# Performance work log

Hardware: AMD Instinct MI355X
Metric: run time of the kernel (lower is better)

## Reference

```python
import jax, jax.numpy as jnp
import numpy as np
from jax import lax


def _lstm_layer(x, Wih, Whh, bih, bhh):
    # x: [B, T, D_in]; PyTorch gate order: i, f, g, o. Returns all hidden states [B, T, H].
    B = x.shape[0]
    H = Whh.shape[1]
    bias = bih + bhh
    # Precompute input projections for all timesteps: [T, B, 4H]
    xg = jnp.einsum('btd,gd->tbg', x, Wih) + bias

    def step(carry, xg_t):
        h, c = carry
        gates = xg_t + h @ Whh.T  # [B, 4H]
        i, f, g, o = jnp.split(gates, 4, axis=-1)
        i = jax.nn.sigmoid(i)
        f = jax.nn.sigmoid(f)
        g = jnp.tanh(g)
        o = jax.nn.sigmoid(o)
        c = f * c + i * g
        h = o * jnp.tanh(c)
        return (h, c), h

    h0 = jnp.zeros((B, H), dtype=x.dtype)
    c0 = jnp.zeros((B, H), dtype=x.dtype)
    (_, _), hs = lax.scan(step, (h0, c0), xg)  # hs: [T, B, H]
    return hs.transpose(1, 0, 2)


def setup_inputs() -> dict:
    key = jax.random.key(0)
    ks = jax.random.split(key, 13)
    B, T, D = 4096, 128, 32
    H1, H2 = 64, 32
    s = lambda n: 1.0 / np.sqrt(n)
    return {
        'x': jax.random.normal(ks[0], (B, T, D), jnp.float32),
        'Wih1': jax.random.uniform(ks[1], (4 * H1, D), jnp.float32, -s(H1), s(H1)),
        'Whh1': jax.random.uniform(ks[2], (4 * H1, H1), jnp.float32, -s(H1), s(H1)),
        'bih1': jax.random.uniform(ks[3], (4 * H1,), jnp.float32, -s(H1), s(H1)),
        'bhh1': jax.random.uniform(ks[4], (4 * H1,), jnp.float32, -s(H1), s(H1)),
        'Wih2': jax.random.uniform(ks[5], (4 * H2, H1), jnp.float32, -s(H2), s(H2)),
        'Whh2': jax.random.uniform(ks[6], (4 * H2, H2), jnp.float32, -s(H2), s(H2)),
        'bih2': jax.random.uniform(ks[7], (4 * H2,), jnp.float32, -s(H2), s(H2)),
        'bhh2': jax.random.uniform(ks[8], (4 * H2,), jnp.float32, -s(H2), s(H2)),
        'fc1_w': jax.random.uniform(ks[9], (16, H2), jnp.float32, -s(H2), s(H2)),
        'fc1_b': jax.random.uniform(ks[10], (16,), jnp.float32, -s(H2), s(H2)),
        'fc2_w': jax.random.uniform(ks[11], (1, 16), jnp.float32, -0.25, 0.25),
        'fc2_b': jax.random.uniform(ks[12], (1,), jnp.float32, -0.25, 0.25),
    }


def reference(x, Wih1, Whh1, bih1, bhh1, Wih2, Whh2, bih2, bhh2, fc1_w, fc1_b, fc2_w, fc2_b):
    out = _lstm_layer(x, Wih1, Whh1, bih1, bhh1)        # [B, T, H1]; dropout = identity (eval)
    out = _lstm_layer(out, Wih2, Whh2, bih2, bhh2)       # [B, T, H2]
    last = out[:, -1, :]                                  # [B, H2]
    h = jax.nn.relu(last @ fc1_w.T + fc1_b)               # [B, 16]
    return h @ fc2_w.T + fc2_b                            # [B, 1]
```

## Files before the change

kernel.cpp:

```cpp
#include <hip/hip_runtime.h>


typedef _Float16 f16;
typedef f16 h2f __attribute__((ext_vector_type(2)));
typedef f16 h8f __attribute__((ext_vector_type(8)));

constexpr int Tt      = 128;
constexpr int NB      = 8;
constexpr int THREADS = 256;

struct __align__(16) Smem {
  float scr[8192];
  h2f h1p[2][32][8];
  h2f h2p[2][16][8];
  h2f xsp[2][16][8];
};

static_assert(sizeof(Smem) <= 80 * 1024, "need 2 blocks/CU");

__device__ __forceinline__ float frcp(float x)   { return __builtin_amdgcn_rcpf(x); }
__device__ __forceinline__ float fsig(float x)   { return frcp(1.0f + __expf(-x)); }
__device__ __forceinline__ float ftanh_(float x) { return 1.0f - 2.0f * frcp(1.0f + __expf(2.0f * x)); }

template<int P>
__device__ __forceinline__ float swz(float v) {
  return __int_as_float(__builtin_amdgcn_ds_swizzle(__float_as_int(v), P));
}

__device__ __forceinline__ h2f pack2(float a, float b) {
  h2f r; r[0] = (f16)a; r[1] = (f16)b; return r;
}

__global__ __launch_bounds__(THREADS, 2)
void lstm_fused(const float* __restrict__ x,
                const float* __restrict__ Wih1, const float* __restrict__ Whh1,
                const float* __restrict__ bih1, const float* __restrict__ bhh1,
                const float* __restrict__ Wih2, const float* __restrict__ Whh2,
                const float* __restrict__ bih2, const float* __restrict__ bhh2,
                const float* __restrict__ fc1w, const float* __restrict__ fc1b,
                const float* __restrict__ fc2w, const float* __restrict__ fc2b,
                float* __restrict__ out)
{
  __shared__ Smem s;
  const int tid = threadIdx.x;
  const int b0  = blockIdx.x * NB;

  const int ks1 = tid & 3;
  const int u1  = tid >> 2;
  const int ks2 = tid & 7;
  const int u2  = tid >> 3;

  h2f w1[12][4];
  h2f w2[6][4];

  auto stage = [&](const float* g, int n) {
    for (int e = tid * 4; e < n; e += THREADS * 4)
      *(float4*)&s.scr[e] = *(const float4*)&g[e];
  };

  stage(Wih1, 8192);
  __syncthreads();
#pragma unroll
  for (int j = 0; j < 4; ++j) {
    int col = 2 * (ks1 + 4 * j);
#pragma unroll
    for (int g = 0; g < 4; ++g)
      w1[j][g] = pack2(s.scr[(g * 64 + u1) * 32 + col],
                       s.scr[(g * 64 + u1) * 32 + col + 1]);
  }
  __syncthreads();

  stage(Whh1, 8192);
  __syncthreads();
#pragma unroll
  for (int j = 4; j < 12; ++j) {
    int col = 2 * (ks1 + 4 * j) - 32;
#pragma unroll
    for (int g = 0; g < 2; ++g)
      w1[j][g] = pack2(s.scr[(g * 64 + u1) * 64 + col],
                       s.scr[(g * 64 + u1) * 64 + col + 1]);
  }
  __syncthreads();

  stage(Whh1 + 8192, 8192);
  __syncthreads();
#pragma unroll
  for (int j = 4; j < 12; ++j) {
    int col = 2 * (ks1 + 4 * j) - 32;
#pragma unroll
    for (int g = 2; g < 4; ++g)
      w1[j][g] = pack2(s.scr[((g - 2) * 64 + u1) * 64 + col],
                       s.scr[((g - 2) * 64 + u1) * 64 + col + 1]);
  }
  __syncthreads();

  stage(Wih2, 8192);
  __syncthreads();
#pragma unroll
  for (int j = 0; j < 4; ++j) {
    int col = 2 * (ks2 + 8 * j);
#pragma unroll
    for (int g = 0; g < 4; ++g)
      w2[j][g] = pack2(s.scr[(g * 32 + u2) * 64 + col],
                       s.scr[(g * 32 + u2) * 64 + col + 1]);
  }
  __syncthreads();

  stage(Whh2, 4096);
  __syncthreads();
#pragma unroll
  for (int j = 4; j < 6; ++j) {
    int col = 2 * (ks2 + 8 * j) - 64;
#pragma unroll
    for (int g = 0; g < 4; ++g)
      w2[j][g] = pack2(s.scr[(g * 32 + u2) * 32 + col],
                       s.scr[(g * 32 + u2) * 32 + col + 1]);
  }

  float bias1[4], bias2[4];
#pragma unroll
  for (int g = 0; g < 4; ++g) {
    bias1[g] = bih1[g * 64 + u1] + bhh1[g * 64 + u1];
    bias2[g] = bih2[g * 32 + u2] + bhh2[g * 32 + u2];
  }

  if (tid < 256) {
    uint* z1 = (uint*)&s.h1p[0][0][0];
    z1[tid] = 0u;
  }
  if (tid < 128) {
    uint* z2 = (uint*)&s.h2p[0][0][0];
    z2[tid] = 0u;
  }

  const int    xb   = tid >> 4;
  const int    xr   = tid & 15;
  const float* xptr = x + (size_t)(b0 + xb) * (Tt * 32) + 2 * xr;
  if (tid < 128) {
    float2 x0 = *(const float2*)xptr;
    s.xsp[0][xr][xb] = pack2(x0.x, x0.y);
  }

  float c1[2] = {0.0f, 0.0f};
  float c2    = 0.0f;

  const bool sA = (ks1 & 1) != 0;
  const bool sB = (ks1 & 2) != 0;
  const bool t0 = (ks2 & 1) != 0;
  const bool t1 = (ks2 & 2) != 0;
  const bool t2 = (ks2 & 4) != 0;

  __syncthreads();

#pragma unroll 1
  for (int t = 0; t < Tt; ++t) {
    const int c = t & 1, n = c ^ 1;

    float2 xpre = make_float2(0.0f, 0.0f);
    if (tid < 128 && t + 1 < Tt) xpre = *(const float2*)(xptr + (size_t)(t + 1) * 32);

    float a[4][8];
#pragma unroll
    for (int g = 0; g < 4; ++g)
#pragma unroll
      for (int b = 0; b < 8; ++b) a[g][b] = 0.0f;

#pragma unroll
    for (int j = 0; j < 12; ++j) {
      const h8f* row = (j < 4) ? (const h8f*)&s.xsp[c][ks1 + 4 * j][0]
                               : (const h8f*)&s.h1p[c][ks1 + 4 * j - 16][0];
      union { h8f v; h2f p[4]; } U0, U1;
      U0.v = row[0];
      U1.v = row[1];
#pragma unroll
      for (int g = 0; g < 4; ++g) {
#pragma unroll
        for (int b = 0; b < 4; ++b)
          a[g][b] = __builtin_amdgcn_fdot2(w1[j][g], U0.p[b], a[g][b], false);
#pragma unroll
        for (int b = 0; b < 4; ++b)
          a[g][4 + b] = __builtin_amdgcn_fdot2(w1[j][g], U1.p[b], a[g][4 + b], false);
      }
    }

    float tot[4][2];
#pragma unroll
    for (int g = 0; g < 4; ++g) {
      float r1[4];
#pragma unroll
      for (int i = 0; i < 4; ++i) {
        float snd  = sA ? a[g][2 * i]     : a[g][2 * i + 1];
        float kept = sA ? a[g][2 * i + 1] : a[g][2 * i];
        r1[i] = kept + swz<0x041F>(snd);
      }
#pragma unroll
      for (int i = 0; i < 2; ++i) {
        float snd  = sB ? r1[2 * i]     : r1[2 * i + 1];
        float kept = sB ? r1[2 * i + 1] : r1[2 * i];
        tot[g][i] = kept + swz<0x081F>(snd);
      }
    }

#pragma unroll
    for (int bb = 0; bb < 2; ++bb) {
      float iv = fsig  (tot[0][bb] + bias1[0]);
      float fv = fsig  (tot[1][bb] + bias1[1]);
      float gv = ftanh_(tot[2][bb] + bias1[2]);
      float ov = fsig  (tot[3][bb] + bias1[3]);
      c1[bb] = fv * c1[bb] + iv * gv;
      float hval = ov * ftanh_(c1[bb]);
      f16* dst = (f16*)&s.h1p[n][u1 >> 1][ks1 + 4 * bb];
      dst[u1 & 1] = (f16)hval;
    }
    __syncthreads();

    if (tid < 128 && t + 1 < Tt) s.xsp[n][xr][xb] = pack2(xpre.x, xpre.y);

    float a2[4][8];
#pragma unroll
    for (int g = 0; g < 4; ++g)
#pragma unroll
      for (int b = 0; b < 8; ++b) a2[g][b] = 0.0f;

#pragma unroll
    for (int j = 0; j < 6; ++j) {
      const h8f* row = (j < 4) ? (const h8f*)&s.h1p[n][ks2 + 8 * j][0]
                               : (const h8f*)&s.h2p[c][ks2 + 8 * j - 32][0];
      union { h8f v; h2f p[4]; } U0, U1;
      U0.v = row[0];
      U1.v = row[1];
#pragma unroll
      for (int g = 0; g < 4; ++g) {
#pragma unroll
        for (int b = 0; b < 4; ++b)
          a2[g][b] = __builtin_amdgcn_fdot2(w2[j][g], U0.p[b], a2[g][b], false);
#pragma unroll
        for (int b = 0; b < 4; ++b)
          a2[g][4 + b] = __builtin_amdgcn_fdot2(w2[j][g], U1.p[b], a2[g][4 + b], false);
      }
    }

    float tot2[4];
#pragma unroll
    for (int g = 0; g < 4; ++g) {
      float r1[4];
#pragma unroll
      for (int i = 0; i < 4; ++i) {
        float snd  = t0 ? a2[g][2 * i]     : a2[g][2 * i + 1];
        float kept = t0 ? a2[g][2 * i + 1] : a2[g][2 * i];
        r1[i] = kept + swz<0x041F>(snd);
      }
      float r2[2];
#pragma unroll
      for (int i = 0; i < 2; ++i) {
        float snd  = t1 ? r1[2 * i]     : r1[2 * i + 1];
        float kept = t1 ? r1[2 * i + 1] : r1[2 * i];
        r2[i] = kept + swz<0x081F>(snd);
      }
      float snd  = t2 ? r2[0] : r2[1];
      float kept = t2 ? r2[1] : r2[0];
      tot2[g] = kept + swz<0x101F>(snd);
    }

    {
      float iv = fsig  (tot2[0] + bias2[0]);
      float fv = fsig  (tot2[1] + bias2[1]);
      float gv = ftanh_(tot2[2] + bias2[2]);
      float ov = fsig  (tot2[3] + bias2[3]);
      c2 = fv * c2 + iv * gv;
      float hval = ov * ftanh_(c2);
      f16* dst = (f16*)&s.h2p[n][u2 >> 1][ks2];
      dst[u2 & 1] = (f16)hval;
    }
    __syncthreads();
  }

  float* fc1out = s.scr;
  if (tid < 128) {
    const int fb = tid >> 4, fu = tid & 15;
    const f16* h2flat = (const f16*)&s.h2p[0][0][0];
    float sacc = fc1b[fu];
#pragma unroll
    for (int k = 0; k < 32; ++k) {
      float hv = (float)h2flat[(k >> 1) * 16 + fb * 2 + (k & 1)];
      sacc = fmaf(fc1w[fu * 32 + k], hv, sacc);
    }
    fc1out[fb * 16 + fu] = fmaxf(sacc, 0.0f);
  }
  __syncthreads();
  if (tid < NB) {
    float o = fc2b[0];
#pragma unroll
    for (int u = 0; u < 16; ++u) o = fmaf(fc2w[u], fc1out[tid * 16 + u], o);
    out[b0 + tid] = o;
  }
}

extern "C" void kernel_launch(void* const* d_in, const int* in_sizes, int n_in,
                              void* d_out, int out_size, void* d_ws, size_t ws_size,
                              hipStream_t stream) {
  const float* x    = (const float*)d_in[0];
  const float* Wih1 = (const float*)d_in[1];
  const float* Whh1 = (const float*)d_in[2];
  const float* bih1 = (const float*)d_in[3];
  const float* bhh1 = (const float*)d_in[4];
  const float* Wih2 = (const float*)d_in[5];
  const float* Whh2 = (const float*)d_in[6];
  const float* bih2 = (const float*)d_in[7];
  const float* bhh2 = (const float*)d_in[8];
  const float* fc1w = (const float*)d_in[9];
  const float* fc1b = (const float*)d_in[10];
  const float* fc2w = (const float*)d_in[11];
  const float* fc2b = (const float*)d_in[12];
  float* out = (float*)d_out;

  hipLaunchKernelGGL(lstm_fused, dim3(4096 / NB), dim3(THREADS), 0, stream,
                     x, Wih1, Whh1, bih1, bhh1,
                     Wih2, Whh2, bih2, bhh2,
                     fc1w, fc1b, fc2w, fc2b, out);
}
```

Baseline: 638.0 us.

## Halve batch per block, preload inputs to shared memory, drop per-step barrier

Each block now handles 4 batch rows instead of 8. Shared memory and launch bounds are resized so 4 blocks fit per CU, and the grid doubles. The whole input sequence for the block is loaded into shared memory as fp16 before the time loop, which removes the per-step global prefetch. The end-of-step barrier is dropped because the double-buffered h1/h2 states and the mid-step barrier already order the accesses. Each thread does half as many dot products per step and the reductions are shortened; the cost is more blocks, more weight staging per batch row, and higher register and occupancy pressure.

```diff
diff --git a/kernel.cpp b/kernel.cpp
--- a/kernel.cpp
+++ b/kernel.cpp
@@ -6,17 +6,17 @@
 typedef f16 h8f __attribute__((ext_vector_type(8)));
 
 constexpr int Tt      = 128;
-constexpr int NB      = 8;
+constexpr int NB      = 4;
 constexpr int THREADS = 256;
 
 struct __align__(16) Smem {
   float scr[8192];
-  h2f h1p[2][32][8];
-  h2f h2p[2][16][8];
-  h2f xsp[2][16][8];
+  h2f h1p[2][32][4];
+  h2f h2p[2][16][4];
+  float fcs[64];
 };
 
-static_assert(sizeof(Smem) <= 80 * 1024, "need 2 blocks/CU");
+static_assert(sizeof(Smem) <= 40 * 1024, "need 4 blocks/CU");
 
 __device__ __forceinline__ float frcp(float x)   { return __builtin_amdgcn_rcpf(x); }
 __device__ __forceinline__ float fsig(float x)   { return frcp(1.0f + __expf(-x)); }
@@ -31,7 +31,7 @@
   h2f r; r[0] = (f16)a; r[1] = (f16)b; return r;
 }
 
-__global__ __launch_bounds__(THREADS, 2)
+__global__ __launch_bounds__(THREADS, 4)
 void lstm_fused(const float* __restrict__ x,
                 const float* __restrict__ Wih1, const float* __restrict__ Whh1,
                 const float* __restrict__ bih1, const float* __restrict__ bhh1,
@@ -116,6 +116,21 @@
       w2[j][g] = pack2(s.scr[(g * 32 + u2) * 32 + col],
                        s.scr[(g * 32 + u2) * 32 + col + 1]);
   }
+  __syncthreads();
+
+  {
+    h2f* xf = (h2f*)s.scr;
+    const int dp = tid & 15;
+    const int t0 = (tid >> 4) & 3;
+    const int xb = tid >> 6;
+    const float* xp = x + (size_t)(b0 + xb) * (Tt * 32) + 2 * dp;
+#pragma unroll 4
+    for (int i = 0; i < 32; ++i) {
+      int t = t0 + 4 * i;
+      float2 v = *(const float2*)(xp + (size_t)t * 32);
+      xf[t * 64 + dp * 4 + xb] = pack2(v.x, v.y);
+    }
+  }
 
   float bias1[4], bias2[4];
 #pragma unroll
@@ -124,31 +139,18 @@
     bias2[g] = bih2[g * 32 + u2] + bhh2[g * 32 + u2];
   }
 
-  if (tid < 256) {
-    uint* z1 = (uint*)&s.h1p[0][0][0];
-    z1[tid] = 0u;
-  }
-  if (tid < 128) {
-    uint* z2 = (uint*)&s.h2p[0][0][0];
-    z2[tid] = 0u;
-  }
-
-  const int    xb   = tid >> 4;
-  const int    xr   = tid & 15;
-  const float* xptr = x + (size_t)(b0 + xb) * (Tt * 32) + 2 * xr;
-  if (tid < 128) {
-    float2 x0 = *(const float2*)xptr;
-    s.xsp[0][xr][xb] = pack2(x0.x, x0.y);
-  }
-
-  float c1[2] = {0.0f, 0.0f};
-  float c2    = 0.0f;
+  if (tid < 128) ((uint*)&s.h1p[0][0][0])[tid] = 0u;
+  if (tid < 64)  ((uint*)&s.h2p[0][0][0])[tid] = 0u;
+
+  float c1 = 0.0f;
+  float c2 = 0.0f;
 
   const bool sA = (ks1 & 1) != 0;
   const bool sB = (ks1 & 2) != 0;
-  const bool t0 = (ks2 & 1) != 0;
-  const bool t1 = (ks2 & 2) != 0;
-  const bool t2 = (ks2 & 4) != 0;
+  const bool t0b = (ks2 & 1) != 0;
+  const bool t1b = (ks2 & 2) != 0;
+
+  const h2f* xf = (const h2f*)s.scr;
 
   __syncthreads();
 
@@ -156,110 +158,82 @@
   for (int t = 0; t < Tt; ++t) {
     const int c = t & 1, n = c ^ 1;
 
-    float2 xpre = make_float2(0.0f, 0.0f);
-    if (tid < 128 && t + 1 < Tt) xpre = *(const float2*)(xptr + (size_t)(t + 1) * 32);
-
-    float a[4][8];
-#pragma unroll
-    for (int g = 0; g < 4; ++g)
-#pragma unroll
-      for (int b = 0; b < 8; ++b) a[g][b] = 0.0f;
+    float a[4][4];
+#pragma unroll
+    for (int g = 0; g < 4; ++g)
+#pragma unroll
+      for (int b = 0; b < 4; ++b) a[g][b] = 0.0f;
 
 #pragma unroll
     for (int j = 0; j < 12; ++j) {
-      const h8f* row = (j < 4) ? (const h8f*)&s.xsp[c][ks1 + 4 * j][0]
-                               : (const h8f*)&s.h1p[c][ks1 + 4 * j - 16][0];
-      union { h8f v; h2f p[4]; } U0, U1;
-      U0.v = row[0];
-      U1.v = row[1];
-#pragma unroll
-      for (int g = 0; g < 4; ++g) {
+      const h8f row = (j < 4) ? *(const h8f*)&xf[t * 64 + (ks1 + 4 * j) * 4]
+                              : *(const h8f*)&s.h1p[c][ks1 + 4 * j - 16][0];
+      union { h8f v; h2f p[4]; } U; U.v = row;
+#pragma unroll
+      for (int g = 0; g < 4; ++g)
 #pragma unroll
         for (int b = 0; b < 4; ++b)
-          a[g][b] = __builtin_amdgcn_fdot2(w1[j][g], U0.p[b], a[g][b], false);
-#pragma unroll
-        for (int b = 0; b < 4; ++b)
-          a[g][4 + b] = __builtin_amdgcn_fdot2(w1[j][g], U1.p[b], a[g][4 + b], false);
-      }
-    }
-
-    float tot[4][2];
+          a[g][b] = __builtin_amdgcn_fdot2(w1[j][g], U.p[b], a[g][b], false);
+    }
+
+    float tot[4];
 #pragma unroll
     for (int g = 0; g < 4; ++g) {
-      float r1[4];
-#pragma unroll
-      for (int i = 0; i < 4; ++i) {
+      float r1[2];
+#pragma unroll
+      for (int i = 0; i < 2; ++i) {
         float snd  = sA ? a[g][2 * i]     : a[g][2 * i + 1];
         float kept = sA ? a[g][2 * i + 1] : a[g][2 * i];
         r1[i] = kept + swz<0x041F>(snd);
       }
+      float snd  = sB ? r1[0] : r1[1];
+      float kept = sB ? r1[1] : r1[0];
+      tot[g] = kept + swz<0x081F>(snd);
+    }
+
+    {
+      float iv = fsig  (tot[0] + bias1[0]);
+      float fv = fsig  (tot[1] + bias1[1]);
+      float gv = ftanh_(tot[2] + bias1[2]);
+      float ov = fsig  (tot[3] + bias1[3]);
+      c1 = fv * c1 + iv * gv;
+      float hval = ov * ftanh_(c1);
+      ((f16*)&s.h1p[n][u1 >> 1][ks1])[u1 & 1] = (f16)hval;
+    }
+    __syncthreads();
+
+    float a2[4][4];
+#pragma unroll
+    for (int g = 0; g < 4; ++g)
+#pragma unroll
+      for (int b = 0; b < 4; ++b) a2[g][b] = 0.0f;
+
+#pragma unroll
+    for (int j = 0; j < 6; ++j) {
+      const h8f row = (j < 4) ? *(const h8f*)&s.h1p[n][ks2 + 8 * j][0]
+                              : *(const h8f*)&s.h2p[c][ks2 + 8 * j - 32][0];
+      union { h8f v; h2f p[4]; } U; U.v = row;
+#pragma unroll
+      for (int g = 0; g < 4; ++g)
+#pragma unroll
+        for (int b = 0; b < 4; ++b)
+          a2[g][b] = __builtin_amdgcn_fdot2(w2[j][g], U.p[b], a2[g][b], false);
+    }
+
+    float tot2[4];
+#pragma unroll
+    for (int g = 0; g < 4; ++g) {
+      float r1[2];
 #pragma unroll
       for (int i = 0; i < 2; ++i) {
-        float snd  = sB ? r1[2 * i]     : r1[2 * i + 1];
-        float kept = sB ? r1[2 * i + 1] : r1[2 * i];
-        tot[g][i] = kept + swz<0x081F>(snd);
-      }
-    }
-
-#pragma unroll
-    for (int bb = 0; bb < 2; ++bb) {
-      float iv = fsig  (tot[0][bb] + bias1[0]);
-      float fv = fsig  (tot[1][bb] + bias1[1]);
-      float gv = ftanh_(tot[2][bb] + bias1[2]);
-      float ov = fsig  (tot[3][bb] + bias1[3]);
-      c1[bb] = fv * c1[bb] + iv * gv;
-      float hval = ov * ftanh_(c1[bb]);
-      f16* dst = (f16*)&s.h1p[n][u1 >> 1][ks1 + 4 * bb];
-      dst[u1 & 1] = (f16)hval;
-    }
-    __syncthreads();
-
-    if (tid < 128 && t + 1 < Tt) s.xsp[n][xr][xb] = pack2(xpre.x, xpre.y);
-
-    float a2[4][8];
-#pragma unroll
-    for (int g = 0; g < 4; ++g)
-#pragma unroll
-      for (int b = 0; b < 8; ++b) a2[g][b] = 0.0f;
-
-#pragma unroll
-    for (int j = 0; j < 6; ++j) {
-      const h8f* row = (j < 4) ? (const h8f*)&s.h1p[n][ks2 + 8 * j][0]
-                               : (const h8f*)&s.h2p[c][ks2 + 8 * j - 32][0];
-      union { h8f v; h2f p[4]; } U0, U1;
-      U0.v = row[0];
-      U1.v = row[1];
-#pragma unroll
-      for (int g = 0; g < 4; ++g) {
-#pragma unroll
-        for (int b = 0; b < 4; ++b)
-          a2[g][b] = __builtin_amdgcn_fdot2(w2[j][g], U0.p[b], a2[g][b], false);
-#pragma unroll
-        for (int b = 0; b < 4; ++b)
-          a2[g][4 + b] = __builtin_amdgcn_fdot2(w2[j][g], U1.p[b], a2[g][4 + b], false);
-      }
-    }
-
-    float tot2[4];
-#pragma unroll
-    for (int g = 0; g < 4; ++g) {
-      float r1[4];
-#pragma unroll
-      for (int i = 0; i < 4; ++i) {
-        float snd  = t0 ? a2[g][2 * i]     : a2[g][2 * i + 1];
-        float kept = t0 ? a2[g][2 * i + 1] : a2[g][2 * i];
+        float snd  = t0b ? a2[g][2 * i]     : a2[g][2 * i + 1];
+        float kept = t0b ? a2[g][2 * i + 1] : a2[g][2 * i];
         r1[i] = kept + swz<0x041F>(snd);
       }
-      float r2[2];
-#pragma unroll
-      for (int i = 0; i < 2; ++i) {
-        float snd  = t1 ? r1[2 * i]     : r1[2 * i + 1];
-        float kept = t1 ? r1[2 * i + 1] : r1[2 * i];
-        r2[i] = kept + swz<0x081F>(snd);
-      }
-      float snd  = t2 ? r2[0] : r2[1];
-      float kept = t2 ? r2[1] : r2[0];
-      tot2[g] = kept + swz<0x101F>(snd);
+      float snd  = t1b ? r1[0] : r1[1];
+      float kept = t1b ? r1[1] : r1[0];
+      float r2 = kept + swz<0x081F>(snd);
+      tot2[g] = r2 + swz<0x101F>(r2);
     }
 
     {
@@ -269,29 +243,27 @@
       float ov = fsig  (tot2[3] + bias2[3]);
       c2 = fv * c2 + iv * gv;
       float hval = ov * ftanh_(c2);
-      f16* dst = (f16*)&s.h2p[n][u2 >> 1][ks2];
-      dst[u2 & 1] = (f16)hval;
-    }
-    __syncthreads();
-  }
-
-  float* fc1out = s.scr;
-  if (tid < 128) {
+      if (ks2 < 4)
+        ((f16*)&s.h2p[n][u2 >> 1][ks2 & 3])[u2 & 1] = (f16)hval;
+    }
+  }
+  __syncthreads();
+
+  if (tid < 64) {
     const int fb = tid >> 4, fu = tid & 15;
-    const f16* h2flat = (const f16*)&s.h2p[0][0][0];
     float sacc = fc1b[fu];
 #pragma unroll
     for (int k = 0; k < 32; ++k) {
-      float hv = (float)h2flat[(k >> 1) * 16 + fb * 2 + (k & 1)];
+      float hv = (float)(((const f16*)&s.h2p[0][k >> 1][fb])[k & 1]);
       sacc = fmaf(fc1w[fu * 32 + k], hv, sacc);
     }
-    fc1out[fb * 16 + fu] = fmaxf(sacc, 0.0f);
+    s.fcs[fb * 16 + fu] = fmaxf(sacc, 0.0f);
   }
   __syncthreads();
   if (tid < NB) {
     float o = fc2b[0];
 #pragma unroll
-    for (int u = 0; u < 16; ++u) o = fmaf(fc2w[u], fc1out[tid * 16 + u], o);
+    for (int u = 0; u < 16; ++u) o = fmaf(fc2w[u], s.fcs[tid * 16 + u], o);
     out[b0 + tid] = o;
   }
 }
```

Measured after the change: 615.9 us. -3.5%, faster.
